# Kernel optimization log

Hardware: AMD Instinct MI355X
Metric: run time of the kernel (lower is better)

Reference implementation:

```python
import jax, jax.numpy as jnp
import numpy as np

H = 12        # num heads
DH = 64       # head dim
W = 8         # window size
WIN2 = W * W  # tokens per window


def _relative_position_index():
    # Swin-style relative position index, [WIN2, WIN2] int array (static).
    coords = np.stack(np.meshgrid(np.arange(W), np.arange(W), indexing='ij'))  # [2,W,W]
    flat = coords.reshape(2, -1)                                               # [2,WIN2]
    rel = flat[:, :, None] - flat[:, None, :]                                  # [2,WIN2,WIN2]
    rel = rel.transpose(1, 2, 0).astype(np.int64)
    rel[..., 0] += W - 1
    rel[..., 1] += W - 1
    rel[..., 0] *= 2 * W - 1
    return rel.sum(-1)  # [WIN2, WIN2]


def setup_inputs() -> dict:
    key = jax.random.key(0)
    ks = jax.random.split(key, 12)
    B, S, D = 128, 256, 768
    scale = 0.02
    return {
        'q': jax.random.normal(ks[0], (B, S, D), jnp.float32),
        'k': jax.random.normal(ks[1], (B, S, D), jnp.float32),
        'v': jax.random.normal(ks[2], (B, S, D), jnp.float32),
        'Wq': jax.random.normal(ks[3], (D, D), jnp.float32) * scale,
        'bq': jnp.zeros((D,), jnp.float32),
        'Wk': jax.random.normal(ks[4], (D, D), jnp.float32) * scale,
        'bk': jnp.zeros((D,), jnp.float32),
        'Wv': jax.random.normal(ks[5], (D, D), jnp.float32) * scale,
        'bv': jnp.zeros((D,), jnp.float32),
        'Wo': jax.random.normal(ks[6], (D, D), jnp.float32) * scale,
        'bo': jnp.zeros((D,), jnp.float32),
        'bias_table': jax.random.normal(ks[7], ((2 * W - 1) ** 2, H), jnp.float32) * scale,
    }


def reference(q, k, v, Wq, bq, Wk, bk, Wv, bv, Wo, bo, bias_table):
    B, S, D = q.shape

    def proj(x, Wt, bt):
        # Linear stores weight as [out, in]; y = x @ W^T + b, then split heads.
        return (x @ Wt.T + bt).reshape(B, S, H, DH).transpose(0, 2, 1, 3)

    qh = proj(q, Wq, bq)  # [B,H,S,DH]
    kh = proj(k, Wk, bk)
    vh = proj(v, Wv, bv)

    scores = jnp.einsum('bhqd,bhkd->bhqk', qh, kh) / np.float32(np.sqrt(DH))

    idx = _relative_position_index()                         # static [WIN2,WIN2]
    bias = bias_table[idx.reshape(-1)].reshape(WIN2, WIN2, H)
    bias = bias.transpose(2, 0, 1)                           # [H,WIN2,WIN2]
    n_contrast = S // WIN2
    bias = jnp.tile(bias, (1, n_contrast, n_contrast))       # [H,S,S]

    probs = jax.nn.softmax(scores + bias[None], axis=-1)     # dropout p=0 (eval)
    ctx = jnp.einsum('bhqk,bhkd->bhqd', probs, vh)
    ctx = ctx.transpose(0, 2, 1, 3).reshape(B, S, D)
    return ctx @ Wo.T + bo
```

## Files before the change

kernel.cpp:

```cpp
#include <hip/hip_runtime.h>


typedef __bf16 bf16;
typedef __bf16 bf16x4 __attribute__((ext_vector_type(4)));
typedef __bf16 bf16x8 __attribute__((ext_vector_type(8)));
typedef float  f32x4  __attribute__((ext_vector_type(4)));

#define MFMA_BF16(a, b, c) __builtin_amdgcn_mfma_f32_16x16x32_bf16((a), (b), (c), 0, 0, 0)

template <typename InT, int MODE>
__global__ __launch_bounds__(256)
void gemm_proj(const InT* __restrict__ X, const float* __restrict__ Wt,
               const float* __restrict__ bias, bf16* __restrict__ outb,
               float* __restrict__ outf)
{
    constexpr int K = 768;
    constexpr int BK = 64;
    constexpr int LDA = 72;
    __shared__ bf16 As[128 * LDA];
    __shared__ bf16 Bs[128 * LDA];

    const int tid  = threadIdx.x;
    const int m0   = blockIdx.x * 128;
    const int n0   = blockIdx.y * 128;
    const int w    = tid >> 6;
    const int lane = tid & 63;
    const int quad = lane >> 4;
    const int l15  = lane & 15;
    const int wr   = (w >> 1) * 64;
    const int wc   = (w & 1) * 64;

    f32x4 acc[4][4] = {};

    for (int kt = 0; kt < K / BK; ++kt) {
        const int k0 = kt * BK;
        __syncthreads();
        if constexpr (sizeof(InT) == 4) {
            #pragma unroll
            for (int i = 0; i < 8; ++i) {
                int idx = i * 256 + tid;
                int row = idx >> 4;
                int c4  = idx & 15;
                f32x4 xv = *(const f32x4*)((const float*)X + (size_t)(m0 + row) * K + k0 + c4 * 4);
                bf16x4 bv;
                bv[0] = (bf16)xv[0]; bv[1] = (bf16)xv[1];
                bv[2] = (bf16)xv[2]; bv[3] = (bf16)xv[3];
                *(bf16x4*)&As[row * LDA + c4 * 4] = bv;
            }
        } else {
            #pragma unroll
            for (int i = 0; i < 4; ++i) {
                int idx = i * 256 + tid;
                int row = idx >> 3;
                int c8  = idx & 7;
                *(bf16x8*)&As[row * LDA + c8 * 8] =
                    *(const bf16x8*)((const bf16*)X + (size_t)(m0 + row) * K + k0 + c8 * 8);
            }
        }
        #pragma unroll
        for (int i = 0; i < 8; ++i) {
            int idx = i * 256 + tid;
            int row = idx >> 4;
            int c4  = idx & 15;
            f32x4 wv = *(const f32x4*)(Wt + (size_t)(n0 + row) * K + k0 + c4 * 4);
            bf16x4 bv;
            bv[0] = (bf16)wv[0]; bv[1] = (bf16)wv[1];
            bv[2] = (bf16)wv[2]; bv[3] = (bf16)wv[3];
            *(bf16x4*)&Bs[row * LDA + c4 * 4] = bv;
        }
        __syncthreads();
        #pragma unroll
        for (int kk = 0; kk < 2; ++kk) {
            bf16x8 af[4], bfr[4];
            #pragma unroll
            for (int mt = 0; mt < 4; ++mt)
                af[mt] = *(const bf16x8*)&As[(wr + mt * 16 + l15) * LDA + kk * 32 + quad * 8];
            #pragma unroll
            for (int nt = 0; nt < 4; ++nt)
                bfr[nt] = *(const bf16x8*)&Bs[(wc + nt * 16 + l15) * LDA + kk * 32 + quad * 8];
            #pragma unroll
            for (int mt = 0; mt < 4; ++mt)
                #pragma unroll
                for (int nt = 0; nt < 4; ++nt)
                    acc[mt][nt] = MFMA_BF16(af[mt], bfr[nt], acc[mt][nt]);
        }
    }

    #pragma unroll
    for (int mt = 0; mt < 4; ++mt) {
        #pragma unroll
        for (int nt = 0; nt < 4; ++nt) {
            int gn = n0 + wc + nt * 16 + l15;
            float bv = bias[gn];
            #pragma unroll
            for (int r = 0; r < 4; ++r) {
                int gm = m0 + wr + mt * 16 + quad * 4 + r;
                float val = acc[mt][nt][r] + bv;
                if constexpr (MODE == 0) {
                    int b = gm >> 8, s = gm & 255;
                    int h = gn >> 6, d = gn & 63;
                    outb[(((size_t)(b * 12 + h) << 8) + s) * 64 + d] = (bf16)val;
                } else {
                    outf[(size_t)gm * 768 + gn] = val;
                }
            }
        }
    }
}

__global__ __launch_bounds__(256)
void attn_kernel(const bf16* __restrict__ qh, const bf16* __restrict__ kh,
                 const bf16* __restrict__ vh, const float* __restrict__ table,
                 bf16* __restrict__ ctx)
{
    constexpr int LD = 72;
    __shared__ bf16  Qs[64 * LD];
    __shared__ bf16  Ks[64 * LD];
    __shared__ bf16  Vt[64 * LD];
    __shared__ bf16  Ps[4 * 16 * LD];
    __shared__ float Bsh[64 * 68];

    const int tid  = threadIdx.x;
    const int qt   = blockIdx.x;
    const int h    = blockIdx.y;
    const int b    = blockIdx.z;
    const int w    = tid >> 6;
    const int lane = tid & 63;
    const int quad = lane >> 4;
    const int l15  = lane & 15;

    const size_t bh = (size_t)(b * 12 + h) * 256 * 64;
    const bf16* Qg = qh + bh + (size_t)qt * 64 * 64;
    const bf16* Kg = kh + bh;
    const bf16* Vg = vh + bh;

    {
        int row = tid >> 2, c0 = (tid & 3) * 16;
        *(bf16x8*)&Qs[row * LD + c0]     = *(const bf16x8*)(Qg + row * 64 + c0);
        *(bf16x8*)&Qs[row * LD + c0 + 8] = *(const bf16x8*)(Qg + row * 64 + c0 + 8);
    }
    {
        int i = tid >> 2, j0 = (tid & 3) * 16;
        int ai = i >> 3, aj = i & 7;
        #pragma unroll
        for (int jj = 0; jj < 16; ++jj) {
            int j = j0 + jj;
            int idx = (ai - (j >> 3) + 7) * 15 + (aj - (j & 7) + 7);
            Bsh[i * 68 + j] = table[idx * 12 + h];
        }
    }

    f32x4 sacc[16] = {};
    bf16x8 qf0, qf1;
    for (int c = 0; c < 4; ++c) {
        __syncthreads();
        {
            int row = tid >> 2, c0 = (tid & 3) * 16;
            const bf16* src = Kg + (size_t)(c * 64 + row) * 64 + c0;
            *(bf16x8*)&Ks[row * LD + c0]     = *(const bf16x8*)(src);
            *(bf16x8*)&Ks[row * LD + c0 + 8] = *(const bf16x8*)(src + 8);
        }
        __syncthreads();
        if (c == 0) {
            qf0 = *(const bf16x8*)&Qs[(w * 16 + l15) * LD + quad * 8];
            qf1 = *(const bf16x8*)&Qs[(w * 16 + l15) * LD + 32 + quad * 8];
        }
        #pragma unroll
        for (int jtl = 0; jtl < 4; ++jtl) {
            bf16x8 kf0 = *(const bf16x8*)&Ks[(jtl * 16 + l15) * LD + quad * 8];
            bf16x8 kf1 = *(const bf16x8*)&Ks[(jtl * 16 + l15) * LD + 32 + quad * 8];
            sacc[c * 4 + jtl] = MFMA_BF16(qf0, kf0, sacc[c * 4 + jtl]);
            sacc[c * 4 + jtl] = MFMA_BF16(qf1, kf1, sacc[c * 4 + jtl]);
        }
    }

    const int browbase = w * 16 + quad * 4;
    float p[16][4];
    #pragma unroll
    for (int jt = 0; jt < 16; ++jt) {
        int jcol = ((jt * 16) & 63) + l15;
        #pragma unroll
        for (int r = 0; r < 4; ++r)
            p[jt][r] = sacc[jt][r] * 0.125f + Bsh[(browbase + r) * 68 + jcol];
    }
    float invl[4];
    #pragma unroll
    for (int r = 0; r < 4; ++r) {
        float m = p[0][r];
        #pragma unroll
        for (int jt = 1; jt < 16; ++jt) m = fmaxf(m, p[jt][r]);
        #pragma unroll
        for (int off = 1; off < 16; off <<= 1)
            m = fmaxf(m, __shfl_xor(m, off, 64));
        float s = 0.f;
        #pragma unroll
        for (int jt = 0; jt < 16; ++jt) {
            p[jt][r] = __expf(p[jt][r] - m);
            s += p[jt][r];
        }
        #pragma unroll
        for (int off = 1; off < 16; off <<= 1)
            s += __shfl_xor(s, off, 64);
        invl[r] = 1.0f / s;
    }

    f32x4 cacc[4] = {};
    bf16* Pw = &Ps[w * 16 * LD];
    for (int c = 0; c < 4; ++c) {
        __syncthreads();
        {
            int row = tid >> 2, c0 = (tid & 3) * 16;
            const bf16* src = Vg + (size_t)(c * 64 + row) * 64 + c0;
            bf16x8 v0 = *(const bf16x8*)(src);
            bf16x8 v1 = *(const bf16x8*)(src + 8);
            #pragma unroll
            for (int d = 0; d < 8; ++d) {
                Vt[(c0 + d) * LD + row]     = v0[d];
                Vt[(c0 + 8 + d) * LD + row] = v1[d];
            }
        }
        #pragma unroll
        for (int jtl = 0; jtl < 4; ++jtl) {
            int jt = c * 4 + jtl;
            #pragma unroll
            for (int r = 0; r < 4; ++r)
                Pw[(quad * 4 + r) * LD + jtl * 16 + l15] = (bf16)(p[jt][r] * invl[r]);
        }
        __syncthreads();
        bf16x8 pf0 = *(const bf16x8*)&Pw[l15 * LD + quad * 8];
        bf16x8 pf1 = *(const bf16x8*)&Pw[l15 * LD + 32 + quad * 8];
        #pragma unroll
        for (int dt = 0; dt < 4; ++dt) {
            bf16x8 vf0 = *(const bf16x8*)&Vt[(dt * 16 + l15) * LD + quad * 8];
            bf16x8 vf1 = *(const bf16x8*)&Vt[(dt * 16 + l15) * LD + 32 + quad * 8];
            cacc[dt] = MFMA_BF16(pf0, vf0, cacc[dt]);
            cacc[dt] = MFMA_BF16(pf1, vf1, cacc[dt]);
        }
    }

    const size_t obase = ((size_t)b * 256) * 768 + (size_t)h * 64;
    #pragma unroll
    for (int dt = 0; dt < 4; ++dt) {
        #pragma unroll
        for (int r = 0; r < 4; ++r) {
            int s = qt * 64 + w * 16 + quad * 4 + r;
            int d = dt * 16 + l15;
            ctx[obase + (size_t)s * 768 + d] = (bf16)cacc[dt][r];
        }
    }
}

extern "C" void kernel_launch(void* const* d_in, const int* in_sizes, int n_in,
                              void* d_out, int out_size, void* d_ws, size_t ws_size,
                              hipStream_t stream) {
    (void)in_sizes; (void)n_in; (void)out_size; (void)ws_size;
    const float* q     = (const float*)d_in[0];
    const float* k     = (const float*)d_in[1];
    const float* v     = (const float*)d_in[2];
    const float* Wq    = (const float*)d_in[3];
    const float* bq    = (const float*)d_in[4];
    const float* Wk    = (const float*)d_in[5];
    const float* bk    = (const float*)d_in[6];
    const float* Wv    = (const float*)d_in[7];
    const float* bv    = (const float*)d_in[8];
    const float* Wo    = (const float*)d_in[9];
    const float* bo    = (const float*)d_in[10];
    const float* table = (const float*)d_in[11];

    const size_t NE = (size_t)128 * 256 * 768;
    bf16* qh  = (bf16*)d_ws;
    bf16* kh  = qh + NE;
    bf16* vh  = kh + NE;
    bf16* ctx = vh + NE;
    float* out = (float*)d_out;

    dim3 gblock(256);
    dim3 ggrid(256, 6);
    gemm_proj<float, 0><<<ggrid, gblock, 0, stream>>>(q, Wq, bq, qh, nullptr);
    gemm_proj<float, 0><<<ggrid, gblock, 0, stream>>>(k, Wk, bk, kh, nullptr);
    gemm_proj<float, 0><<<ggrid, gblock, 0, stream>>>(v, Wv, bv, vh, nullptr);

    dim3 agrid(4, 12, 128);
    attn_kernel<<<agrid, gblock, 0, stream>>>(qh, kh, vh, table, ctx);

    gemm_proj<bf16, 1><<<ggrid, gblock, 0, stream>>>(ctx, Wo, bo, nullptr, out);
}
```

Baseline: 812.0 us.

## Merge QKV projections, use direct global-to-LDS loads, pre-transpose V

Combines the three input projections into one launch indexed by grid z, loads tiles into LDS with global_load_lds (fp32 activations kept in LDS and converted at fragment read), and adds a separate kernel that transposes V so attention can load it directly. The relative bias is stored as bf16 in LDS, the LDS row padding is dropped, and the ctx buffer reuses the vh workspace. These aim to cut per-thread conversion and scatter work and launch count. In exchange they add an extra transpose pass, double the LDS footprint for A, and may add bank conflicts from the unpadded layouts.

```diff
diff --git a/kernel.cpp b/kernel.cpp
--- a/kernel.cpp
+++ b/kernel.cpp
@@ -2,23 +2,40 @@
 
 
 typedef __bf16 bf16;
-typedef __bf16 bf16x4 __attribute__((ext_vector_type(4)));
 typedef __bf16 bf16x8 __attribute__((ext_vector_type(8)));
 typedef float  f32x4  __attribute__((ext_vector_type(4)));
 
 #define MFMA_BF16(a, b, c) __builtin_amdgcn_mfma_f32_16x16x32_bf16((a), (b), (c), 0, 0, 0)
 
-template <typename InT, int MODE>
+__device__ __forceinline__ void gld16(const void* g, void* l) {
+    __builtin_amdgcn_global_load_lds(
+        (const __attribute__((address_space(1))) void*)g,
+        (__attribute__((address_space(3))) void*)l, 16, 0, 0);
+}
+
+__device__ __forceinline__ bf16x8 pack8(f32x4 lo, f32x4 hi) {
+    bf16x8 r;
+    r[0] = (bf16)lo[0]; r[1] = (bf16)lo[1]; r[2] = (bf16)lo[2]; r[3] = (bf16)lo[3];
+    r[4] = (bf16)hi[0]; r[5] = (bf16)hi[1]; r[6] = (bf16)hi[2]; r[7] = (bf16)hi[3];
+    return r;
+}
+
 __global__ __launch_bounds__(256)
-void gemm_proj(const InT* __restrict__ X, const float* __restrict__ Wt,
-               const float* __restrict__ bias, bf16* __restrict__ outb,
-               float* __restrict__ outf)
+void gemm_qkv(const float* __restrict__ q, const float* __restrict__ k,
+              const float* __restrict__ v,
+              const float* __restrict__ Wq, const float* __restrict__ Wk,
+              const float* __restrict__ Wv,
+              const float* __restrict__ bq, const float* __restrict__ bk,
+              const float* __restrict__ bv, bf16* __restrict__ outbase)
 {
-    constexpr int K = 768;
-    constexpr int BK = 64;
-    constexpr int LDA = 72;
-    __shared__ bf16 As[128 * LDA];
-    __shared__ bf16 Bs[128 * LDA];
+    __shared__ float As[128 * 64];
+    __shared__ bf16  Bs[128 * 64];
+
+    const int z = blockIdx.z;
+    const float* X    = (z == 0) ? q  : (z == 1) ? k  : v;
+    const float* Wt   = (z == 0) ? Wq : (z == 1) ? Wk : Wv;
+    const float* bias = (z == 0) ? bq : (z == 1) ? bk : bv;
+    bf16* out = outbase + (size_t)z * 25165824;
 
     const int tid  = threadIdx.x;
     const int m0   = blockIdx.x * 128;
@@ -32,52 +49,35 @@
 
     f32x4 acc[4][4] = {};
 
-    for (int kt = 0; kt < K / BK; ++kt) {
-        const int k0 = kt * BK;
-        __syncthreads();
-        if constexpr (sizeof(InT) == 4) {
-            #pragma unroll
-            for (int i = 0; i < 8; ++i) {
-                int idx = i * 256 + tid;
-                int row = idx >> 4;
-                int c4  = idx & 15;
-                f32x4 xv = *(const f32x4*)((const float*)X + (size_t)(m0 + row) * K + k0 + c4 * 4);
-                bf16x4 bv;
-                bv[0] = (bf16)xv[0]; bv[1] = (bf16)xv[1];
-                bv[2] = (bf16)xv[2]; bv[3] = (bf16)xv[3];
-                *(bf16x4*)&As[row * LDA + c4 * 4] = bv;
-            }
-        } else {
-            #pragma unroll
-            for (int i = 0; i < 4; ++i) {
-                int idx = i * 256 + tid;
-                int row = idx >> 3;
-                int c8  = idx & 7;
-                *(bf16x8*)&As[row * LDA + c8 * 8] =
-                    *(const bf16x8*)((const bf16*)X + (size_t)(m0 + row) * K + k0 + c8 * 8);
-            }
-        }
-        #pragma unroll
-        for (int i = 0; i < 8; ++i) {
-            int idx = i * 256 + tid;
-            int row = idx >> 4;
-            int c4  = idx & 15;
-            f32x4 wv = *(const f32x4*)(Wt + (size_t)(n0 + row) * K + k0 + c4 * 4);
-            bf16x4 bv;
-            bv[0] = (bf16)wv[0]; bv[1] = (bf16)wv[1];
-            bv[2] = (bf16)wv[2]; bv[3] = (bf16)wv[3];
-            *(bf16x4*)&Bs[row * LDA + c4 * 4] = bv;
+    for (int kt = 0; kt < 12; ++kt) {
+        const int k0 = kt * 64;
+        __syncthreads();
+        #pragma unroll
+        for (int p = 0; p < 8; ++p) {
+            int g = p * 256 + tid;
+            gld16(X + (size_t)(m0 + (g >> 4)) * 768 + k0 + (g & 15) * 4,
+                  (char*)As + g * 16);
+        }
+        #pragma unroll
+        for (int p = 0; p < 4; ++p) {
+            int g = p * 256 + tid;
+            const float* src = Wt + (size_t)(n0 + (g >> 3)) * 768 + k0 + (g & 7) * 8;
+            f32x4 lo = *(const f32x4*)src;
+            f32x4 hi = *(const f32x4*)(src + 4);
+            *(bf16x8*)&Bs[g * 8] = pack8(lo, hi);
         }
         __syncthreads();
         #pragma unroll
         for (int kk = 0; kk < 2; ++kk) {
             bf16x8 af[4], bfr[4];
             #pragma unroll
-            for (int mt = 0; mt < 4; ++mt)
-                af[mt] = *(const bf16x8*)&As[(wr + mt * 16 + l15) * LDA + kk * 32 + quad * 8];
+            for (int mt = 0; mt < 4; ++mt) {
+                const float* ap = &As[(wr + mt * 16 + l15) * 64 + kk * 32 + quad * 8];
+                af[mt] = pack8(*(const f32x4*)ap, *(const f32x4*)(ap + 4));
+            }
             #pragma unroll
             for (int nt = 0; nt < 4; ++nt)
-                bfr[nt] = *(const bf16x8*)&Bs[(wc + nt * 16 + l15) * LDA + kk * 32 + quad * 8];
+                bfr[nt] = *(const bf16x8*)&Bs[(wc + nt * 16 + l15) * 64 + kk * 32 + quad * 8];
             #pragma unroll
             for (int mt = 0; mt < 4; ++mt)
                 #pragma unroll
@@ -92,33 +92,127 @@
         for (int nt = 0; nt < 4; ++nt) {
             int gn = n0 + wc + nt * 16 + l15;
             float bv = bias[gn];
+            int h = gn >> 6, d = gn & 63;
             #pragma unroll
             for (int r = 0; r < 4; ++r) {
                 int gm = m0 + wr + mt * 16 + quad * 4 + r;
-                float val = acc[mt][nt][r] + bv;
-                if constexpr (MODE == 0) {
-                    int b = gm >> 8, s = gm & 255;
-                    int h = gn >> 6, d = gn & 63;
-                    outb[(((size_t)(b * 12 + h) << 8) + s) * 64 + d] = (bf16)val;
-                } else {
-                    outf[(size_t)gm * 768 + gn] = val;
-                }
+                int b = gm >> 8, s = gm & 255;
+                out[(((size_t)(b * 12 + h) << 8) + s) * 64 + d] = (bf16)(acc[mt][nt][r] + bv);
             }
         }
+    }
+}
+
+__global__ __launch_bounds__(256)
+void gemm_out(const bf16* __restrict__ X, const float* __restrict__ Wt,
+              const float* __restrict__ bias, float* __restrict__ out)
+{
+    __shared__ bf16 As[128 * 64];
+    __shared__ bf16 Bs[128 * 64];
+
+    const int tid  = threadIdx.x;
+    const int m0   = blockIdx.x * 128;
+    const int n0   = blockIdx.y * 128;
+    const int w    = tid >> 6;
+    const int lane = tid & 63;
+    const int quad = lane >> 4;
+    const int l15  = lane & 15;
+    const int wr   = (w >> 1) * 64;
+    const int wc   = (w & 1) * 64;
+
+    f32x4 acc[4][4] = {};
+
+    for (int kt = 0; kt < 12; ++kt) {
+        const int k0 = kt * 64;
+        __syncthreads();
+        #pragma unroll
+        for (int p = 0; p < 4; ++p) {
+            int g = p * 256 + tid;
+            gld16(X + (size_t)(m0 + (g >> 3)) * 768 + k0 + (g & 7) * 8,
+                  (char*)As + g * 16);
+        }
+        #pragma unroll
+        for (int p = 0; p < 4; ++p) {
+            int g = p * 256 + tid;
+            const float* src = Wt + (size_t)(n0 + (g >> 3)) * 768 + k0 + (g & 7) * 8;
+            *(bf16x8*)&Bs[g * 8] = pack8(*(const f32x4*)src, *(const f32x4*)(src + 4));
+        }
+        __syncthreads();
+        #pragma unroll
+        for (int kk = 0; kk < 2; ++kk) {
+            bf16x8 af[4], bfr[4];
+            #pragma unroll
+            for (int mt = 0; mt < 4; ++mt)
+                af[mt] = *(const bf16x8*)&As[(wr + mt * 16 + l15) * 64 + kk * 32 + quad * 8];
+            #pragma unroll
+            for (int nt = 0; nt < 4; ++nt)
+                bfr[nt] = *(const bf16x8*)&Bs[(wc + nt * 16 + l15) * 64 + kk * 32 + quad * 8];
+            #pragma unroll
+            for (int mt = 0; mt < 4; ++mt)
+                #pragma unroll
+                for (int nt = 0; nt < 4; ++nt)
+                    acc[mt][nt] = MFMA_BF16(af[mt], bfr[nt], acc[mt][nt]);
+        }
+    }
+
+    #pragma unroll
+    for (int mt = 0; mt < 4; ++mt) {
+        #pragma unroll
+        for (int nt = 0; nt < 4; ++nt) {
+            int gn = n0 + wc + nt * 16 + l15;
+            float bv = bias[gn];
+            #pragma unroll
+            for (int r = 0; r < 4; ++r) {
+                int gm = m0 + wr + mt * 16 + quad * 4 + r;
+                out[(size_t)gm * 768 + gn] = acc[mt][nt][r] + bv;
+            }
+        }
+    }
+}
+
+__global__ __launch_bounds__(256)
+void transpose_v(const bf16* __restrict__ vh, bf16* __restrict__ vt)
+{
+    __shared__ bf16 Ts[64 * 65];
+    const int qt = blockIdx.x, h = blockIdx.y, b = blockIdx.z;
+    const bf16* src = vh + ((size_t)(b * 12 + h) * 256 + qt * 64) * 64;
+    bf16* dst = vt + (size_t)(b * 12 + h) * 64 * 256;
+
+    const int tid = threadIdx.x;
+    {
+        int row = tid >> 2, c0 = (tid & 3) * 16;
+        bf16x8 v0 = *(const bf16x8*)(src + row * 64 + c0);
+        bf16x8 v1 = *(const bf16x8*)(src + row * 64 + c0 + 8);
+        #pragma unroll
+        for (int i = 0; i < 8; ++i) {
+            Ts[row * 65 + c0 + i]     = v0[i];
+            Ts[row * 65 + c0 + 8 + i] = v1[i];
+        }
+    }
+    __syncthreads();
+    {
+        int d = tid >> 2, j0 = (tid & 3) * 16;
+        bf16x8 o0, o1;
+        #pragma unroll
+        for (int i = 0; i < 8; ++i) {
+            o0[i] = Ts[(j0 + i) * 65 + d];
+            o1[i] = Ts[(j0 + 8 + i) * 65 + d];
+        }
+        *(bf16x8*)(dst + (size_t)d * 256 + qt * 64 + j0)     = o0;
+        *(bf16x8*)(dst + (size_t)d * 256 + qt * 64 + j0 + 8) = o1;
     }
 }
 
 __global__ __launch_bounds__(256)
 void attn_kernel(const bf16* __restrict__ qh, const bf16* __restrict__ kh,
-                 const bf16* __restrict__ vh, const float* __restrict__ table,
+                 const bf16* __restrict__ vt, const float* __restrict__ table,
                  bf16* __restrict__ ctx)
 {
-    constexpr int LD = 72;
-    __shared__ bf16  Qs[64 * LD];
-    __shared__ bf16  Ks[64 * LD];
-    __shared__ bf16  Vt[64 * LD];
-    __shared__ bf16  Ps[4 * 16 * LD];
-    __shared__ float Bsh[64 * 68];
+    __shared__ bf16 Qs[64 * 64];
+    __shared__ bf16 Ks[64 * 64];
+    __shared__ bf16 Vs[64 * 64];
+    __shared__ bf16 Ps[4 * 16 * 72];
+    __shared__ bf16 Bsh[64 * 68];
 
     const int tid  = threadIdx.x;
     const int qt   = blockIdx.x;
@@ -130,14 +224,14 @@
     const int l15  = lane & 15;
 
     const size_t bh = (size_t)(b * 12 + h) * 256 * 64;
-    const bf16* Qg = qh + bh + (size_t)qt * 64 * 64;
-    const bf16* Kg = kh + bh;
-    const bf16* Vg = vh + bh;
-
-    {
-        int row = tid >> 2, c0 = (tid & 3) * 16;
-        *(bf16x8*)&Qs[row * LD + c0]     = *(const bf16x8*)(Qg + row * 64 + c0);
-        *(bf16x8*)&Qs[row * LD + c0 + 8] = *(const bf16x8*)(Qg + row * 64 + c0 + 8);
+    const bf16* Qg  = qh + bh + (size_t)qt * 64 * 64;
+    const bf16* Kg  = kh + bh;
+    const bf16* Vtg = vt + bh;
+
+    #pragma unroll
+    for (int p = 0; p < 2; ++p) {
+        int g = p * 256 + tid;
+        gld16(Qg + (size_t)(g >> 3) * 64 + (g & 7) * 8, (char*)Qs + g * 16);
     }
     {
         int i = tid >> 2, j0 = (tid & 3) * 16;
@@ -146,7 +240,7 @@
         for (int jj = 0; jj < 16; ++jj) {
             int j = j0 + jj;
             int idx = (ai - (j >> 3) + 7) * 15 + (aj - (j & 7) + 7);
-            Bsh[i * 68 + j] = table[idx * 12 + h];
+            Bsh[i * 68 + j] = (bf16)table[idx * 12 + h];
         }
     }
 
@@ -154,21 +248,20 @@
     bf16x8 qf0, qf1;
     for (int c = 0; c < 4; ++c) {
         __syncthreads();
-        {
-            int row = tid >> 2, c0 = (tid & 3) * 16;
-            const bf16* src = Kg + (size_t)(c * 64 + row) * 64 + c0;
-            *(bf16x8*)&Ks[row * LD + c0]     = *(const bf16x8*)(src);
-            *(bf16x8*)&Ks[row * LD + c0 + 8] = *(const bf16x8*)(src + 8);
+        #pragma unroll
+        for (int p = 0; p < 2; ++p) {
+            int g = p * 256 + tid;
+            gld16(Kg + (size_t)(c * 64 + (g >> 3)) * 64 + (g & 7) * 8, (char*)Ks + g * 16);
         }
         __syncthreads();
         if (c == 0) {
-            qf0 = *(const bf16x8*)&Qs[(w * 16 + l15) * LD + quad * 8];
-            qf1 = *(const bf16x8*)&Qs[(w * 16 + l15) * LD + 32 + quad * 8];
+            qf0 = *(const bf16x8*)&Qs[(w * 16 + l15) * 64 + quad * 8];
+            qf1 = *(const bf16x8*)&Qs[(w * 16 + l15) * 64 + 32 + quad * 8];
         }
         #pragma unroll
         for (int jtl = 0; jtl < 4; ++jtl) {
-            bf16x8 kf0 = *(const bf16x8*)&Ks[(jtl * 16 + l15) * LD + quad * 8];
-            bf16x8 kf1 = *(const bf16x8*)&Ks[(jtl * 16 + l15) * LD + 32 + quad * 8];
+            bf16x8 kf0 = *(const bf16x8*)&Ks[(jtl * 16 + l15) * 64 + quad * 8];
+            bf16x8 kf1 = *(const bf16x8*)&Ks[(jtl * 16 + l15) * 64 + 32 + quad * 8];
             sacc[c * 4 + jtl] = MFMA_BF16(qf0, kf0, sacc[c * 4 + jtl]);
             sacc[c * 4 + jtl] = MFMA_BF16(qf1, kf1, sacc[c * 4 + jtl]);
         }
@@ -181,7 +274,7 @@
         int jcol = ((jt * 16) & 63) + l15;
         #pragma unroll
         for (int r = 0; r < 4; ++r)
-            p[jt][r] = sacc[jt][r] * 0.125f + Bsh[(browbase + r) * 68 + jcol];
+            p[jt][r] = sacc[jt][r] * 0.125f + (float)Bsh[(browbase + r) * 68 + jcol];
     }
     float invl[4];
     #pragma unroll
@@ -205,34 +298,28 @@
     }
 
     f32x4 cacc[4] = {};
-    bf16* Pw = &Ps[w * 16 * LD];
+    bf16* Pw = &Ps[w * 16 * 72];
     for (int c = 0; c < 4; ++c) {
         __syncthreads();
-        {
-            int row = tid >> 2, c0 = (tid & 3) * 16;
-            const bf16* src = Vg + (size_t)(c * 64 + row) * 64 + c0;
-            bf16x8 v0 = *(const bf16x8*)(src);
-            bf16x8 v1 = *(const bf16x8*)(src + 8);
-            #pragma unroll
-            for (int d = 0; d < 8; ++d) {
-                Vt[(c0 + d) * LD + row]     = v0[d];
-                Vt[(c0 + 8 + d) * LD + row] = v1[d];
-            }
+        #pragma unroll
+        for (int pp = 0; pp < 2; ++pp) {
+            int g = pp * 256 + tid;
+            gld16(Vtg + (size_t)(g >> 3) * 256 + c * 64 + (g & 7) * 8, (char*)Vs + g * 16);
         }
         #pragma unroll
         for (int jtl = 0; jtl < 4; ++jtl) {
             int jt = c * 4 + jtl;
             #pragma unroll
             for (int r = 0; r < 4; ++r)
-                Pw[(quad * 4 + r) * LD + jtl * 16 + l15] = (bf16)(p[jt][r] * invl[r]);
-        }
-        __syncthreads();
-        bf16x8 pf0 = *(const bf16x8*)&Pw[l15 * LD + quad * 8];
-        bf16x8 pf1 = *(const bf16x8*)&Pw[l15 * LD + 32 + quad * 8];
+                Pw[(quad * 4 + r) * 72 + jtl * 16 + l15] = (bf16)(p[jt][r] * invl[r]);
+        }
+        __syncthreads();
+        bf16x8 pf0 = *(const bf16x8*)&Pw[l15 * 72 + quad * 8];
+        bf16x8 pf1 = *(const bf16x8*)&Pw[l15 * 72 + 32 + quad * 8];
         #pragma unroll
         for (int dt = 0; dt < 4; ++dt) {
-            bf16x8 vf0 = *(const bf16x8*)&Vt[(dt * 16 + l15) * LD + quad * 8];
-            bf16x8 vf1 = *(const bf16x8*)&Vt[(dt * 16 + l15) * LD + 32 + quad * 8];
+            bf16x8 vf0 = *(const bf16x8*)&Vs[(dt * 16 + l15) * 64 + quad * 8];
+            bf16x8 vf1 = *(const bf16x8*)&Vs[(dt * 16 + l15) * 64 + 32 + quad * 8];
             cacc[dt] = MFMA_BF16(pf0, vf0, cacc[dt]);
             cacc[dt] = MFMA_BF16(pf1, vf1, cacc[dt]);
         }
@@ -271,17 +358,13 @@
     bf16* qh  = (bf16*)d_ws;
     bf16* kh  = qh + NE;
     bf16* vh  = kh + NE;
-    bf16* ctx = vh + NE;
+    bf16* vt  = vh + NE;
+    bf16* ctx = vh;
     float* out = (float*)d_out;
 
-    dim3 gblock(256);
-    dim3 ggrid(256, 6);
-    gemm_proj<float, 0><<<ggrid, gblock, 0, stream>>>(q, Wq, bq, qh, nullptr);
-    gemm_proj<float, 0><<<ggrid, gblock, 0, stream>>>(k, Wk, bk, kh, nullptr);
-    gemm_proj<float, 0><<<ggrid, gblock, 0, stream>>>(v, Wv, bv, vh, nullptr);
-
-    dim3 agrid(4, 12, 128);
-    attn_kernel<<<agrid, gblock, 0, stream>>>(qh, kh, vh, table, ctx);
-
-    gemm_proj<bf16, 1><<<ggrid, gblock, 0, stream>>>(ctx, Wo, bo, nullptr, out);
-}
+    dim3 blk(256);
+    gemm_qkv<<<dim3(256, 6, 3), blk, 0, stream>>>(q, k, v, Wq, Wk, Wv, bq, bk, bv, qh);
+    transpose_v<<<dim3(4, 12, 128), blk, 0, stream>>>(vh, vt);
+    attn_kernel<<<dim3(4, 12, 128), blk, 0, stream>>>(qh, kh, vt, table, ctx);
+    gemm_out<<<dim3(256, 6), blk, 0, stream>>>(ctx, Wo, bo, out);
+}
```

Measured after the change: 780.8 us. -3.8%, faster.
